# Performance work log

Hardware: AMD Instinct MI355X
Metric: run time of the kernel (lower is better)

## Reference

```python
import jax, jax.numpy as jnp
import numpy as np

N = 50000      # nodes
E = 800000     # edges
IN_DIM = 128
HID = 64
OUT = 2


def _sage_conv(h, src, dst, Wl, bl, Wr, n_nodes):
    """PyG SAGEConv (mean aggr): lin_l(mean_{j in N(i)} h_j) + lin_r(h_i).
    Messages flow src -> dst. lin_r has no bias (PyG default)."""
    msg = h[src]                                             # [E, d]
    agg = jax.ops.segment_sum(msg, dst, num_segments=n_nodes)  # [N, d]
    cnt = jax.ops.segment_sum(jnp.ones((msg.shape[0],), h.dtype), dst,
                              num_segments=n_nodes)          # [N]
    agg = agg / jnp.maximum(cnt, 1.0)[:, None]               # mean, zero-deg safe
    return agg @ Wl + bl + h @ Wr


def setup_inputs() -> dict:
    key = jax.random.key(0)
    ks = jax.random.split(key, 12)
    def lin(k, fan_in, fan_out):
        s = 1.0 / np.sqrt(fan_in)
        return jax.random.uniform(k, (fan_in, fan_out), jnp.float32, -s, s)
    x = jax.random.normal(ks[0], (N, IN_DIM), jnp.float32)
    edge_index = jax.random.randint(ks[1], (2, E), 0, N, jnp.int64)
    return {
        "x": x,
        "edge_index": edge_index,
        # conv1
        "W1l": lin(ks[2], IN_DIM, HID),
        "b1l": jnp.zeros((HID,), jnp.float32),
        "W1r": lin(ks[3], IN_DIM, HID),
        # conv2
        "W2l": lin(ks[4], HID, HID),
        "b2l": jnp.zeros((HID,), jnp.float32),
        "W2r": lin(ks[5], HID, HID),
        # edge MLP
        "Wm1": lin(ks[6], 2 * HID, HID),
        "bm1": jnp.zeros((HID,), jnp.float32),
        "Wm2": lin(ks[7], HID, OUT),
        "bm2": jnp.zeros((OUT,), jnp.float32),
    }


def reference(x, edge_index, W1l, b1l, W1r, W2l, b2l, W2r, Wm1, bm1, Wm2, bm2):
    src, dst = edge_index[0], edge_index[1]
    h = jax.nn.relu(_sage_conv(x, src, dst, W1l, b1l, W1r, N))   # [N, HID]
    h = jax.nn.relu(_sage_conv(h, src, dst, W2l, b2l, W2r, N))   # [N, HID]
    edge_rep = jnp.concatenate([h[src], h[dst]], axis=1)          # [E, 2*HID]
    hidden = jax.nn.relu(edge_rep @ Wm1 + bm1)                    # [E, HID]
    return hidden @ Wm2 + bm2                                     # [E, OUT]
```

## Files before the change

kernel.cpp:

```cpp
#include <hip/hip_runtime.h>

#define N_NODES 50000
#define N_EDGES 800000

#define BVALS 64
#define NBUK ((N_NODES + BVALS - 1) / BVALS)
#define PAD 16
#define CHUNK 4096
#define NSB ((N_EDGES + CHUNK - 1) / CHUNK)
#define BCAP 2048
#define PREPB 128

typedef __attribute__((ext_vector_type(8))) short bf16x8;
typedef __attribute__((ext_vector_type(4))) float f32x4;


__device__ __forceinline__ float bf2f(unsigned short u) {
    return __uint_as_float(((unsigned)u) << 16);
}
__device__ __forceinline__ unsigned short f2bf(float f) {
    unsigned u = __float_as_uint(f);
    u += 0x7FFFu + ((u >> 16) & 1u);
    return (unsigned short)(u >> 16);
}
__device__ __forceinline__ unsigned pack2bf(float a, float b) {
    return (unsigned)f2bf(a) | ((unsigned)f2bf(b) << 16);
}
__device__ __forceinline__ float lobf(int w) {
    return __uint_as_float(((unsigned)w) << 16);
}
__device__ __forceinline__ float hibf(int w) {
    return __uint_as_float(((unsigned)w) & 0xFFFF0000u);
}
__device__ __forceinline__ void stv(float* p, float v) { *p = v; }
__device__ __forceinline__ void stv(unsigned short* p, float v) { *p = f2bf(v); }

__device__ __forceinline__ void add8(float* a, int4 v) {
    a[0] += lobf(v.x); a[1] += hibf(v.x);
    a[2] += lobf(v.y); a[3] += hibf(v.y);
    a[4] += lobf(v.z); a[5] += hibf(v.z);
    a[6] += lobf(v.w); a[7] += hibf(v.w);
}


__global__ __launch_bounds__(256) void count_prep_kernel(
        const int* __restrict__ ei, int* __restrict__ bhist,
        const float* __restrict__ W1l, const float* __restrict__ W1r,
        const float* __restrict__ W2l, const float* __restrict__ W2r,
        const float* __restrict__ Wm1,
        unsigned short* __restrict__ wt1, unsigned short* __restrict__ wt2,
        unsigned short* __restrict__ wtm, int E) {
    __shared__ int hist[NBUK];
    int t = threadIdx.x;
    if (blockIdx.x >= NSB) {
        int id = (blockIdx.x - NSB) * 256 + t;
        if (id < 128 * 128) {
            int k = id >> 7, c = id & 127;
            float v = (c < 64) ? W1l[k * 64 + c] : W1r[k * 64 + (c - 64)];
            wt1[c * 128 + k] = f2bf(v);
        } else if (id < 128 * 128 + 64 * 128) {
            int j = id - 128 * 128;
            int k = j >> 7, c = j & 127;
            float v = (c < 64) ? W2l[k * 64 + c] : W2r[k * 64 + (c - 64)];
            wt2[c * 64 + k] = f2bf(v);
        } else if (id < 128 * 128 + 64 * 128 + 64 * 128) {
            int j = id - 128 * 128 - 64 * 128;
            int k = j >> 7, c = j & 127;
            float v = (c < 64) ? Wm1[k * 64 + c] : Wm1[(64 + k) * 64 + (c - 64)];
            wtm[c * 64 + k] = f2bf(v);
        }
        return;
    }
    for (int h = t; h < NBUK; h += 256) hist[h] = 0;
    __syncthreads();
    int e0 = blockIdx.x * CHUNK;
    int ne = min(CHUNK, E - e0);
    for (int i = t; i < ne; i += 256)
        atomicAdd(&hist[ei[E + e0 + i] >> 6], 1);
    __syncthreads();
    for (int h = t; h < NBUK; h += 256)
        bhist[blockIdx.x * NBUK + h] = hist[h];
}

__global__ __launch_bounds__(1024) void scan_bcnt_kernel(
        const int* __restrict__ bhist, int* __restrict__ bofs,
        int* __restrict__ gcur_pad) {
    __shared__ int lds[1024];
    int t = threadIdx.x;
    int v = 0;
    if (t < NBUK)
        for (int b = 0; b < NSB; ++b) v += bhist[b * NBUK + t];
    lds[t] = v;
    __syncthreads();
    for (int off = 1; off < 1024; off <<= 1) {
        int u = (t >= off) ? lds[t - off] : 0;
        __syncthreads();
        lds[t] += u;
        __syncthreads();
    }
    if (t <= NBUK) bofs[t] = lds[t] - ((t < NBUK) ? v : 0);
    if (t < NBUK) gcur_pad[t * PAD] = lds[t] - v;
}


template<int K>
__device__ __forceinline__ void stage_w(
        const unsigned short* __restrict__ WT, unsigned short* w_lds, int t) {
    constexpr int KP = K + 8;
    for (int idx = t; idx < 128 * K / 8; idx += 256) {
        int f = idx * 8;
        int r = f / K, c = f % K;
        *(int4*)&w_lds[r * KP + c] = *(const int4*)&WT[r * K + c];
    }
}

template<int K, typename T0, typename T1>
__device__ __forceinline__ void mfma_tile(
        const unsigned short* a_lds, const unsigned short* w_lds,
        int t, int n0, T0* __restrict__ C0, T1* __restrict__ C1, int N) {
    constexpr int KP = K + 8;
    int w = t >> 6, l = t & 63;
    int lr = l & 15;
    int lk = (l >> 4) * 8;

    f32x4 acc[8];
#pragma unroll
    for (int i = 0; i < 8; ++i) acc[i] = (f32x4)(0.f);

#pragma unroll
    for (int kc = 0; kc < K / 32; ++kc) {
        bf16x8 af = *(const bf16x8*)&a_lds[(w * 16 + lr) * KP + kc * 32 + lk];
#pragma unroll
        for (int ct = 0; ct < 8; ++ct) {
            bf16x8 bfr = *(const bf16x8*)&w_lds[(ct * 16 + lr) * KP + kc * 32 + lk];
            acc[ct] = __builtin_amdgcn_mfma_f32_16x16x32_bf16(af, bfr, acc[ct], 0, 0, 0);
        }
    }

    int orow = n0 + w * 16 + (l >> 4) * 4;
#pragma unroll
    for (int ct = 0; ct < 4; ++ct) {
#pragma unroll
        for (int r = 0; r < 4; ++r) {
            if (orow + r < N) stv(&C0[(size_t)(orow + r) * 64 + ct * 16 + lr], acc[ct][r]);
        }
    }
#pragma unroll
    for (int ct = 4; ct < 8; ++ct) {
#pragma unroll
        for (int r = 0; r < 4; ++r) {
            if (orow + r < N) stv(&C1[(size_t)(orow + r) * 64 + (ct - 4) * 16 + lr], acc[ct][r]);
        }
    }
}


__global__ __launch_bounds__(256) void scatter_gemm1_kernel(
        const int* __restrict__ ei, int* __restrict__ gcur_pad,
        unsigned int* __restrict__ bpk,
        const float* __restrict__ x, const unsigned short* __restrict__ wt1,
        unsigned short* __restrict__ C0, unsigned short* __restrict__ C1,
        int N, int E) {
    __shared__ __align__(16) char smem[52224];
    int t = threadIdx.x;

    if (blockIdx.x < NSB) {
        unsigned int* pk = (unsigned int*)smem;
        int* hist  = (int*)(pk + CHUNK);
        int* lbase = hist + NBUK;
        for (int h = t; h < NBUK; h += 256) hist[h] = 0;
        __syncthreads();
        int e0 = blockIdx.x * CHUNK;
        int ne = min(CHUNK, E - e0);
        for (int i = t; i < ne; i += 256) {
            unsigned s = (unsigned)ei[e0 + i];
            unsigned d = (unsigned)ei[E + e0 + i];
            pk[i] = (d << 16) | s;
            atomicAdd(&hist[d >> 6], 1);
        }
        __syncthreads();
        for (int h = t; h < NBUK; h += 256) {
            int c = hist[h];
            lbase[h] = c ? atomicAdd(&gcur_pad[h * PAD], c) : 0;
            hist[h] = 0;
        }
        __syncthreads();
        for (int i = t; i < ne; i += 256) {
            unsigned v = pk[i];
            int h = (v >> 16) >> 6;
            int idx = atomicAdd(&hist[h], 1);
            bpk[lbase[h] + idx] = v;
        }
        return;
    }

    constexpr int K = 128, KP = K + 8;
    unsigned short* a_lds = (unsigned short*)smem;
    unsigned short* w_lds = a_lds + 64 * KP;
    int n0 = (blockIdx.x - NSB) * 64;

    for (int idx = t; idx < 64 * K / 4; idx += 256) {
        int f = idx * 4;
        int r = f / K, c = f % K;
        float4 v = make_float4(0.f, 0.f, 0.f, 0.f);
        if (n0 + r < N) v = *(const float4*)&x[(size_t)(n0 + r) * K + c];
        ushort4 o;
        o.x = f2bf(v.x); o.y = f2bf(v.y); o.z = f2bf(v.z); o.w = f2bf(v.w);
        *(ushort4*)&a_lds[r * KP + c] = o;
    }
    stage_w<K>(wt1, w_lds, t);
    __syncthreads();
    mfma_tile<K>(a_lds, w_lds, t, n0, C0, C1, N);
}


__global__ __launch_bounds__(256) void sort_agg_gemm_kernel(
        const unsigned int* __restrict__ bpk, const int* __restrict__ bofs,
        int* __restrict__ rowptr, int* __restrict__ elist,
        const unsigned short* __restrict__ P, const unsigned short* __restrict__ R,
        const float* __restrict__ bias,
        const unsigned short* __restrict__ WT,
        unsigned short* __restrict__ C0, unsigned short* __restrict__ C1, int N) {
    constexpr int K = 64, KP = K + 8;
    __shared__ unsigned int pk[BCAP];
    __shared__ unsigned short srt[BCAP];
    __shared__ int sc[BVALS];
    __shared__ int ex[BVALS + 1];
    __shared__ int cur[BVALS];
    __shared__ unsigned short a_lds[64 * KP];
    __shared__ unsigned short w_lds[128 * KP];
    int t = threadIdx.x;
    int b = blockIdx.x;
    int n0 = b * 64;

    stage_w<K>(WT, w_lds, t);

    int e0 = bofs[b];
    int nb = min(bofs[b + 1] - e0, BCAP);

    if (t < BVALS) sc[t] = 0;
    __syncthreads();
    for (int i = t; i < nb; i += 256) {
        unsigned v = bpk[e0 + i];
        pk[i] = v;
        atomicAdd(&sc[(v >> 16) & 63], 1);
    }
    __syncthreads();
    int hv = (t < BVALS) ? sc[t] : 0;
#pragma unroll
    for (int off = 1; off < BVALS; off <<= 1) {
        int u = (t < BVALS && t >= off) ? sc[t - off] : 0;
        __syncthreads();
        if (t < BVALS) sc[t] += u;
        __syncthreads();
    }
    if (t < BVALS) {
        int e = sc[t] - hv;
        ex[t] = e;
        cur[t] = e;
        if (t == BVALS - 1) ex[BVALS] = nb;
        int n = n0 + t;
        if (n <= N_NODES) rowptr[n] = e0 + e;
    }
    __syncthreads();
    for (int i = t; i < nb; i += 256) {
        unsigned v = pk[i];
        int pos = atomicAdd(&cur[(v >> 16) & 63], 1);
        srt[pos] = (unsigned short)(v & 0xFFFF);
        elist[e0 + pos] = (int)(v & 0xFFFF);
    }
    __syncthreads();

    int l8 = t & 7;
    int nr = t >> 3;
    float4 b0 = *(const float4*)&bias[l8 * 8];
    float4 b1 = *(const float4*)&bias[l8 * 8 + 4];

#pragma unroll
    for (int half = 0; half < 2; ++half) {
        int r = half * 32 + nr;
        int n = n0 + r;
        float a0[8] = {0.f, 0.f, 0.f, 0.f, 0.f, 0.f, 0.f, 0.f};
        float a1[8] = {0.f, 0.f, 0.f, 0.f, 0.f, 0.f, 0.f, 0.f};
        int rs = ex[r], re = ex[r + 1];
        int p = rs;
        for (; p + 2 <= re; p += 2) {
            int sA = srt[p], sB = srt[p + 1];
            int4 vA = *(const int4*)&P[(size_t)sA * 64 + l8 * 8];
            int4 vB = *(const int4*)&P[(size_t)sB * 64 + l8 * 8];
            add8(a0, vA);
            add8(a1, vB);
        }
        if (p < re) {
            int sA = srt[p];
            add8(a0, *(const int4*)&P[(size_t)sA * 64 + l8 * 8]);
        }
        int4 o = make_int4(0, 0, 0, 0);
        if (n < N) {
            float inv = 1.0f / fmaxf((float)(re - rs), 1.0f);
            int4 rv = *(const int4*)&R[(size_t)n * 64 + l8 * 8];
            float h0 = fmaxf(fmaf(a0[0] + a1[0], inv, b0.x + lobf(rv.x)), 0.f);
            float h1 = fmaxf(fmaf(a0[1] + a1[1], inv, b0.y + hibf(rv.x)), 0.f);
            float h2 = fmaxf(fmaf(a0[2] + a1[2], inv, b0.z + lobf(rv.y)), 0.f);
            float h3 = fmaxf(fmaf(a0[3] + a1[3], inv, b0.w + hibf(rv.y)), 0.f);
            float h4 = fmaxf(fmaf(a0[4] + a1[4], inv, b1.x + lobf(rv.z)), 0.f);
            float h5 = fmaxf(fmaf(a0[5] + a1[5], inv, b1.y + hibf(rv.z)), 0.f);
            float h6 = fmaxf(fmaf(a0[6] + a1[6], inv, b1.z + lobf(rv.w)), 0.f);
            float h7 = fmaxf(fmaf(a0[7] + a1[7], inv, b1.w + hibf(rv.w)), 0.f);
            o.x = pack2bf(h0, h1); o.y = pack2bf(h2, h3);
            o.z = pack2bf(h4, h5); o.w = pack2bf(h6, h7);
        }
        *(int4*)&a_lds[r * KP + l8 * 8] = o;
    }
    __syncthreads();
    mfma_tile<K>(a_lds, w_lds, t, n0, C0, C1, N);
}


__global__ __launch_bounds__(256) void agg_gemm_kernel(
        const unsigned short* __restrict__ P, const unsigned short* __restrict__ R,
        const float* __restrict__ bias,
        const int* __restrict__ rowptr, const int* __restrict__ elist,
        const unsigned short* __restrict__ WT,
        unsigned short* __restrict__ C0, unsigned short* __restrict__ C1, int N) {
    constexpr int K = 64, KP = K + 8;
    __shared__ unsigned short a_lds[64 * KP];
    __shared__ unsigned short w_lds[128 * KP];
    int t = threadIdx.x;
    int n0 = blockIdx.x * 64;

    stage_w<K>(WT, w_lds, t);

    int l8 = t & 7;
    int nr = t >> 3;
    float4 b0 = *(const float4*)&bias[l8 * 8];
    float4 b1 = *(const float4*)&bias[l8 * 8 + 4];

#pragma unroll
    for (int half = 0; half < 2; ++half) {
        int r = half * 32 + nr;
        int n = n0 + r;
        float a0[8] = {0.f, 0.f, 0.f, 0.f, 0.f, 0.f, 0.f, 0.f};
        float a1[8] = {0.f, 0.f, 0.f, 0.f, 0.f, 0.f, 0.f, 0.f};
        int r0 = 0, r1 = 0;
        if (n < N) { r0 = rowptr[n]; r1 = rowptr[n + 1]; }
        int p = r0;
        for (; p + 2 <= r1; p += 2) {
            int sA = elist[p], sB = elist[p + 1];
            int4 vA = *(const int4*)&P[(size_t)sA * 64 + l8 * 8];
            int4 vB = *(const int4*)&P[(size_t)sB * 64 + l8 * 8];
            add8(a0, vA);
            add8(a1, vB);
        }
        if (p < r1) {
            int sA = elist[p];
            add8(a0, *(const int4*)&P[(size_t)sA * 64 + l8 * 8]);
        }
        int4 o = make_int4(0, 0, 0, 0);
        if (n < N) {
            float inv = 1.0f / fmaxf((float)(r1 - r0), 1.0f);
            int4 rv = *(const int4*)&R[(size_t)n * 64 + l8 * 8];
            float h0 = fmaxf(fmaf(a0[0] + a1[0], inv, b0.x + lobf(rv.x)), 0.f);
            float h1 = fmaxf(fmaf(a0[1] + a1[1], inv, b0.y + hibf(rv.x)), 0.f);
            float h2 = fmaxf(fmaf(a0[2] + a1[2], inv, b0.z + lobf(rv.y)), 0.f);
            float h3 = fmaxf(fmaf(a0[3] + a1[3], inv, b0.w + hibf(rv.y)), 0.f);
            float h4 = fmaxf(fmaf(a0[4] + a1[4], inv, b1.x + lobf(rv.z)), 0.f);
            float h5 = fmaxf(fmaf(a0[5] + a1[5], inv, b1.y + hibf(rv.z)), 0.f);
            float h6 = fmaxf(fmaf(a0[6] + a1[6], inv, b1.z + lobf(rv.w)), 0.f);
            float h7 = fmaxf(fmaf(a0[7] + a1[7], inv, b1.w + hibf(rv.w)), 0.f);
            o.x = pack2bf(h0, h1); o.y = pack2bf(h2, h3);
            o.z = pack2bf(h4, h5); o.w = pack2bf(h6, h7);
        }
        *(int4*)&a_lds[r * KP + l8 * 8] = o;
    }
    __syncthreads();
    mfma_tile<K>(a_lds, w_lds, t, n0, C0, C1, N);
}


__global__ __launch_bounds__(256) void edge_out_kernel(
        const unsigned short* __restrict__ Pa, const unsigned short* __restrict__ Pb,
        const int* __restrict__ ei,
        const float* __restrict__ bm1,
        const float* __restrict__ Wm2, const float* __restrict__ bm2,
        float* __restrict__ out, int E) {
    int t = threadIdx.x;
    int l8 = t & 7;
    int eg = t >> 3;
    int base = blockIdx.x * 128 + eg;

    float4 wA = *(const float4*)&Wm2[l8 * 16];
    float4 wB = *(const float4*)&Wm2[l8 * 16 + 4];
    float4 wC = *(const float4*)&Wm2[l8 * 16 + 8];
    float4 wD = *(const float4*)&Wm2[l8 * 16 + 12];
    float4 bbA = *(const float4*)&bm1[l8 * 8];
    float4 bbB = *(const float4*)&bm1[l8 * 8 + 4];
    float ob0 = bm2[0], ob1 = bm2[1];

#pragma unroll
    for (int it = 0; it < 4; ++it) {
        int e = base + it * 32;
        int s = ei[e];
        int d = ei[E + e];
        int4 ua = *(const int4*)&Pa[(size_t)s * 64 + l8 * 8];
        int4 ub = *(const int4*)&Pb[(size_t)d * 64 + l8 * 8];
        float h0 = fmaxf(lobf(ua.x) + lobf(ub.x) + bbA.x, 0.f);
        float h1 = fmaxf(hibf(ua.x) + hibf(ub.x) + bbA.y, 0.f);
        float h2 = fmaxf(lobf(ua.y) + lobf(ub.y) + bbA.z, 0.f);
        float h3 = fmaxf(hibf(ua.y) + hibf(ub.y) + bbA.w, 0.f);
        float h4 = fmaxf(lobf(ua.z) + lobf(ub.z) + bbB.x, 0.f);
        float h5 = fmaxf(hibf(ua.z) + hibf(ub.z) + bbB.y, 0.f);
        float h6 = fmaxf(lobf(ua.w) + lobf(ub.w) + bbB.z, 0.f);
        float h7 = fmaxf(hibf(ua.w) + hibf(ub.w) + bbB.w, 0.f);
        float s0 = h0 * wA.x + h1 * wA.z + h2 * wB.x + h3 * wB.z
                 + h4 * wC.x + h5 * wC.z + h6 * wD.x + h7 * wD.z;
        float s1 = h0 * wA.y + h1 * wA.w + h2 * wB.y + h3 * wB.w
                 + h4 * wC.y + h5 * wC.w + h6 * wD.y + h7 * wD.w;
#pragma unroll
        for (int off = 4; off >= 1; off >>= 1) {
            s0 += __shfl_xor(s0, off, 64);
            s1 += __shfl_xor(s1, off, 64);
        }
        if (l8 == 0) {
            *(float2*)&out[(size_t)e * 2] = make_float2(s0 + ob0, s1 + ob1);
        }
    }
}


extern "C" void kernel_launch(void* const* d_in, const int* in_sizes, int n_in,
                              void* d_out, int out_size, void* d_ws, size_t ws_size,
                              hipStream_t stream) {
    const float* x   = (const float*)d_in[0];
    const int*   ei  = (const int*)d_in[1];
    const float* W1l = (const float*)d_in[2];
    const float* b1l = (const float*)d_in[3];
    const float* W1r = (const float*)d_in[4];
    const float* W2l = (const float*)d_in[5];
    const float* b2l = (const float*)d_in[6];
    const float* W2r = (const float*)d_in[7];
    const float* Wm1 = (const float*)d_in[8];
    const float* bm1 = (const float*)d_in[9];
    const float* Wm2 = (const float*)d_in[10];
    const float* bm2 = (const float*)d_in[11];
    float* out = (float*)d_out;

    const int N = N_NODES, E = N_EDGES;

    float* B0 = (float*)d_ws;
    float* B1 = B0 + (size_t)N * 64;
    float* B2 = B1 + (size_t)N * 64;
    unsigned short* B3h = (unsigned short*)(B2 + (size_t)N * 64);
    int* rowptr   = (int*)(B3h + (size_t)N * 64);
    int* elist    = rowptr + N + 1;
    int* bofs     = elist + E;
    int* gcur_pad = bofs + NBUK + 1;
    int* bhist    = gcur_pad + NBUK * PAD;
    unsigned short* wt1 = (unsigned short*)(bhist + NSB * NBUK);
    unsigned short* wt2 = wt1 + 128 * 128;
    unsigned short* wtm = wt2 + 128 * 64;
    unsigned int* bpk = (unsigned int*)B2;

    unsigned short* B0h = (unsigned short*)B0;
    unsigned short* B1h = (unsigned short*)B1;
    unsigned short* B2h = (unsigned short*)B2;

    count_prep_kernel<<<NSB + PREPB, 256, 0, stream>>>(
        ei, bhist, W1l, W1r, W2l, W2r, Wm1, wt1, wt2, wtm, E);
    scan_bcnt_kernel<<<1, 1024, 0, stream>>>(bhist, bofs, gcur_pad);

    scatter_gemm1_kernel<<<NSB + (N + 63) / 64, 256, 0, stream>>>(
        ei, gcur_pad, bpk, x, wt1, B0h, B1h, N, E);

    sort_agg_gemm_kernel<<<NBUK, 256, 0, stream>>>(
        bpk, bofs, rowptr, elist, B0h, B1h, b1l, wt2, B2h, B1h, N);

    agg_gemm_kernel<<<(N + 63) / 64, 256, 0, stream>>>(
        B2h, B1h, b2l, rowptr, elist, wtm, B0h, B3h, N);

    edge_out_kernel<<<E / 128, 256, 0, stream>>>(B0h, B3h, ei, bm1, Wm2, bm2, out, E);
}
```

Before: 126.5 us.

## Process edge MLP in destination-sorted order and scatter outputs by original edge id

```diff
diff --git a/kernel.cpp b/kernel.cpp
--- a/kernel.cpp
+++ b/kernel.cpp
@@ -157,7 +157,7 @@
 
 __global__ __launch_bounds__(256) void scatter_gemm1_kernel(
         const int* __restrict__ ei, int* __restrict__ gcur_pad,
-        unsigned int* __restrict__ bpk,
+        unsigned int* __restrict__ bpk, int* __restrict__ bpk_id,
         const float* __restrict__ x, const unsigned short* __restrict__ wt1,
         unsigned short* __restrict__ C0, unsigned short* __restrict__ C1,
         int N, int E) {
@@ -190,6 +190,7 @@
             int h = (v >> 16) >> 6;
             int idx = atomicAdd(&hist[h], 1);
             bpk[lbase[h] + idx] = v;
+            bpk_id[lbase[h] + idx] = e0 + i;
         }
         return;
     }
@@ -215,8 +216,9 @@
 
 
 __global__ __launch_bounds__(256) void sort_agg_gemm_kernel(
-        const unsigned int* __restrict__ bpk, const int* __restrict__ bofs,
-        int* __restrict__ rowptr, int* __restrict__ elist,
+        const unsigned int* __restrict__ bpk, const int* __restrict__ bpk_id,
+        const int* __restrict__ bofs,
+        int* __restrict__ rowptr, int* __restrict__ elist, int* __restrict__ eidx,
         const unsigned short* __restrict__ P, const unsigned short* __restrict__ R,
         const float* __restrict__ bias,
         const unsigned short* __restrict__ WT,
@@ -267,7 +269,8 @@
         unsigned v = pk[i];
         int pos = atomicAdd(&cur[(v >> 16) & 63], 1);
         srt[pos] = (unsigned short)(v & 0xFFFF);
-        elist[e0 + pos] = (int)(v & 0xFFFF);
+        elist[e0 + pos] = (int)v;
+        eidx[e0 + pos] = bpk_id[e0 + i];
     }
     __syncthreads();
 
@@ -346,14 +349,14 @@
         if (n < N) { r0 = rowptr[n]; r1 = rowptr[n + 1]; }
         int p = r0;
         for (; p + 2 <= r1; p += 2) {
-            int sA = elist[p], sB = elist[p + 1];
+            int sA = elist[p] & 0xFFFF, sB = elist[p + 1] & 0xFFFF;
             int4 vA = *(const int4*)&P[(size_t)sA * 64 + l8 * 8];
             int4 vB = *(const int4*)&P[(size_t)sB * 64 + l8 * 8];
             add8(a0, vA);
             add8(a1, vB);
         }
         if (p < r1) {
-            int sA = elist[p];
+            int sA = elist[p] & 0xFFFF;
             add8(a0, *(const int4*)&P[(size_t)sA * 64 + l8 * 8]);
         }
         int4 o = make_int4(0, 0, 0, 0);
@@ -380,7 +383,7 @@
 
 __global__ __launch_bounds__(256) void edge_out_kernel(
         const unsigned short* __restrict__ Pa, const unsigned short* __restrict__ Pb,
-        const int* __restrict__ ei,
+        const int* __restrict__ elist, const int* __restrict__ eidx,
         const float* __restrict__ bm1,
         const float* __restrict__ Wm2, const float* __restrict__ bm2,
         float* __restrict__ out, int E) {
@@ -399,9 +402,11 @@
 
 #pragma unroll
     for (int it = 0; it < 4; ++it) {
-        int e = base + it * 32;
-        int s = ei[e];
-        int d = ei[E + e];
+        int p = base + it * 32;
+        int v = elist[p];
+        int oid = eidx[p];
+        int s = v & 0xFFFF;
+        int d = ((unsigned)v) >> 16;
         int4 ua = *(const int4*)&Pa[(size_t)s * 64 + l8 * 8];
         int4 ub = *(const int4*)&Pb[(size_t)d * 64 + l8 * 8];
         float h0 = fmaxf(lobf(ua.x) + lobf(ub.x) + bbA.x, 0.f);
@@ -422,7 +427,7 @@
             s1 += __shfl_xor(s1, off, 64);
         }
         if (l8 == 0) {
-            *(float2*)&out[(size_t)e * 2] = make_float2(s0 + ob0, s1 + ob1);
+            *(float2*)&out[(size_t)oid * 2] = make_float2(s0 + ob0, s1 + ob1);
         }
     }
 }
@@ -451,32 +456,35 @@
     float* B1 = B0 + (size_t)N * 64;
     float* B2 = B1 + (size_t)N * 64;
     unsigned short* B3h = (unsigned short*)(B2 + (size_t)N * 64);
-    int* rowptr   = (int*)(B3h + (size_t)N * 64);
+    unsigned short* B4h = B3h + (size_t)N * 64;
+    int* rowptr   = (int*)(B4h + (size_t)N * 64);
     int* elist    = rowptr + N + 1;
-    int* bofs     = elist + E;
+    int* eidx     = elist + E;
+    int* bofs     = eidx + E;
     int* gcur_pad = bofs + NBUK + 1;
     int* bhist    = gcur_pad + NBUK * PAD;
     unsigned short* wt1 = (unsigned short*)(bhist + NSB * NBUK);
     unsigned short* wt2 = wt1 + 128 * 128;
     unsigned short* wtm = wt2 + 128 * 64;
     unsigned int* bpk = (unsigned int*)B2;
+    int* bpk_id = (int*)(bpk + E);
 
     unsigned short* B0h = (unsigned short*)B0;
     unsigned short* B1h = (unsigned short*)B1;
-    unsigned short* B2h = (unsigned short*)B2;
 
     count_prep_kernel<<<NSB + PREPB, 256, 0, stream>>>(
         ei, bhist, W1l, W1r, W2l, W2r, Wm1, wt1, wt2, wtm, E);
     scan_bcnt_kernel<<<1, 1024, 0, stream>>>(bhist, bofs, gcur_pad);
 
     scatter_gemm1_kernel<<<NSB + (N + 63) / 64, 256, 0, stream>>>(
-        ei, gcur_pad, bpk, x, wt1, B0h, B1h, N, E);
+        ei, gcur_pad, bpk, bpk_id, x, wt1, B0h, B1h, N, E);
 
     sort_agg_gemm_kernel<<<NBUK, 256, 0, stream>>>(
-        bpk, bofs, rowptr, elist, B0h, B1h, b1l, wt2, B2h, B1h, N);
+        bpk, bpk_id, bofs, rowptr, elist, eidx, B0h, B1h, b1l, wt2, B4h, B1h, N);
 
     agg_gemm_kernel<<<(N + 63) / 64, 256, 0, stream>>>(
-        B2h, B1h, b2l, rowptr, elist, wtm, B0h, B3h, N);
-
-    edge_out_kernel<<<E / 128, 256, 0, stream>>>(B0h, B3h, ei, bm1, Wm2, bm2, out, E);
-}
+        B4h, B1h, b2l, rowptr, elist, wtm, B0h, B3h, N);
+
+    edge_out_kernel<<<E / 128, 256, 0, stream>>>(
+        B0h, B3h, elist, eidx, bm1, Wm2, bm2, out, E);
+}
```

New measurement: 136.0 us. 1.07x slower.
